# Kernel optimization log

Measured on AMD Instinct MI355X. Metric: run time of the kernel, lower is better.

The kernel has to match this reference:

```python
import jax, jax.numpy as jnp
import numpy as np

N_NODES = 50000
N_EDGES = 800000
F_IN = 256
HID = 64
HEADS = 4
NEG_SLOPE = 0.2


def setup_inputs() -> dict:
    key = jax.random.key(0)
    ks = jax.random.split(key, 12)
    x = jax.random.normal(ks[0], (N_NODES, F_IN), dtype=jnp.float32)
    src = jax.random.randint(ks[1], (N_EDGES,), 0, N_NODES)
    dst = jax.random.randint(ks[2], (N_EDGES,), 0, N_NODES)
    s0 = 1.0 / np.sqrt(F_IN)
    s1 = 1.0 / np.sqrt(HEADS * HID)
    W0 = jax.random.normal(ks[3], (F_IN, HEADS * HID), dtype=jnp.float32) * s0
    a_l0 = jax.random.normal(ks[4], (HEADS, HID), dtype=jnp.float32) * s1
    a_r0 = jax.random.normal(ks[5], (HEADS, HID), dtype=jnp.float32) * s1
    b0 = jnp.zeros((HEADS * HID,), dtype=jnp.float32)
    W1 = jax.random.normal(ks[6], (HEADS * HID, HEADS * HID), dtype=jnp.float32) * s1
    a_l1 = jax.random.normal(ks[7], (HEADS, HID), dtype=jnp.float32) * s1
    a_r1 = jax.random.normal(ks[8], (HEADS, HID), dtype=jnp.float32) * s1
    b1 = jnp.zeros((HEADS * HID,), dtype=jnp.float32)
    return {"x": x, "src": src, "dst": dst,
            "W0": W0, "a_l0": a_l0, "a_r0": a_r0, "b0": b0,
            "W1": W1, "a_l1": a_l1, "a_r1": a_r1, "b1": b1}


def _gat_layer(h, src, dst, W, a_l, a_r, b):
    # h: [N, F_in] -> feat: [N, H, D]
    feat = (h @ W).reshape(h.shape[0], HEADS, HID)
    el = jnp.sum(feat * a_l, axis=-1)  # [N, H]
    er = jnp.sum(feat * a_r, axis=-1)  # [N, H]
    e = jax.nn.leaky_relu(el[src] + er[dst], NEG_SLOPE)  # [E, H]
    # per-destination edge softmax (numerically stable)
    m = jax.ops.segment_max(e, dst, num_segments=N_NODES)  # [N, H]
    ex = jnp.exp(e - m[dst])
    s = jax.ops.segment_sum(ex, dst, num_segments=N_NODES)  # [N, H]
    alpha = ex / jnp.maximum(s[dst], 1e-9)  # [E, H]
    msg = feat[src] * alpha[:, :, None]  # [E, H, D]
    rst = jax.ops.segment_sum(msg, dst, num_segments=N_NODES)  # [N, H, D]
    rst = rst + b.reshape(1, HEADS, HID)
    return jax.nn.elu(rst)


def reference(x, src, dst, W0, a_l0, a_r0, b0, W1, a_l1, a_r1, b1):
    h = _gat_layer(x, src, dst, W0, a_l0, a_r0, b0)  # [N, H, D]
    h = h.reshape(N_NODES, HEADS * HID)              # flatten(1)
    h = _gat_layer(h, src, dst, W1, a_l1, a_r1, b1)  # [N, H, D]
    # list of per-head outputs h[:, i]
    return tuple(h[:, i] for i in range(HEADS))
```

## Files before the change

### kernel.cpp

```cpp
#include <hip/hip_runtime.h>
#include <math.h>

#define N_NODES 50000
#define N_EDGES 800000
#define HEADS 4
#define HID 64
#define FDIM 256
#define SCAN_CHUNK 1024
#define SCAN_NB ((N_NODES + SCAN_CHUNK - 1) / SCAN_CHUNK)

typedef __attribute__((ext_vector_type(8))) _Float16 half8;
typedef __attribute__((ext_vector_type(4))) _Float16 half4;
typedef __attribute__((ext_vector_type(4))) float f32x4;


__global__ __launch_bounds__(256) void scan_local(const int* __restrict__ counts,
                                                  int* __restrict__ offs,
                                                  int* __restrict__ bsum, int n) {
    __shared__ int part[256];
    const int b = blockIdx.x, t = threadIdx.x;
    const int base = b * SCAN_CHUNK + t * 4;
    int v[4];
#pragma unroll
    for (int j = 0; j < 4; j++) {
        int idx = base + j;
        v[j] = (idx < n) ? counts[idx] : 0;
    }
    int s0 = v[0], s1 = s0 + v[1], s2 = s1 + v[2], s3 = s2 + v[3];
    part[t] = s3;
    __syncthreads();
    for (int off = 1; off < 256; off <<= 1) {
        int x = (t >= off) ? part[t - off] : 0;
        __syncthreads();
        part[t] += x;
        __syncthreads();
    }
    int prefix = (t > 0) ? part[t - 1] : 0;
    int e[4] = {prefix, prefix + s0, prefix + s1, prefix + s2};
#pragma unroll
    for (int j = 0; j < 4; j++) {
        int idx = base + j;
        if (idx < n) offs[idx] = e[j];
    }
    if (t == 255) bsum[b] = part[255];
}

__global__ __launch_bounds__(64) void scan_bsum(int* __restrict__ bsum,
                                                int* __restrict__ offs, int nb, int n) {
    int lane = threadIdx.x;
    int own = (lane < nb) ? bsum[lane] : 0;
    int v = own;
    for (int off = 1; off < 64; off <<= 1) {
        int x = __shfl_up(v, off);
        if (lane >= off) v += x;
    }
    if (lane < nb) bsum[lane] = v - own;
    if (lane == nb - 1) offs[n] = v;
}

__global__ __launch_bounds__(256) void scan_add(int* __restrict__ offs,
                                                const int* __restrict__ bsum, int n) {
    const int b = blockIdx.x;
    const int p = bsum[b];
    const int base = b * SCAN_CHUNK + threadIdx.x * 4;
#pragma unroll
    for (int j = 0; j < 4; j++) {
        int idx = base + j;
        if (idx < n) offs[idx] += p;
    }
}

__global__ __launch_bounds__(256) void scatter_kernel(const int* __restrict__ src,
                                                      const int* __restrict__ dst,
                                                      const int* __restrict__ offs,
                                                      int* __restrict__ cursor,
                                                      int* __restrict__ csr_src, int E) {
    int i = blockIdx.x * blockDim.x + threadIdx.x;
    if (i < E) {
        int d = dst[i];
        int p = offs[d] + atomicAdd(&cursor[d], 1);
        csr_src[p] = src[i];
    }
}


__global__ __launch_bounds__(256) void wcast_kernel(const float* __restrict__ W0,
                                                    const float* __restrict__ W1,
                                                    _Float16* __restrict__ wt0,
                                                    _Float16* __restrict__ wt1) {
    const float* W = blockIdx.y ? W1 : W0;
    _Float16* wt = blockIdx.y ? wt1 : wt0;
    int n = blockIdx.x * 16 + (threadIdx.x >> 4);
    int k0 = (threadIdx.x & 15) * 16;
    for (int j = 0; j < 16; j++)
        wt[n * FDIM + k0 + j] = (_Float16)W[(k0 + j) * FDIM + n];
}

template <int A32, int DO_HIST>
__global__ __launch_bounds__(512) void mfma_gemm(const _Float16* __restrict__ A16,
                                                 const float* __restrict__ Af,
                                                 const _Float16* __restrict__ Bt,
                                                 const float* __restrict__ al,
                                                 const float* __restrict__ ar,
                                                 _Float16* __restrict__ feat16,
                                                 float* __restrict__ el,
                                                 float* __restrict__ er,
                                                 const int* __restrict__ dst,
                                                 int* __restrict__ counts) {
    __shared__ _Float16 ash[64 * 32];
    __shared__ _Float16 bsh[256 * 32];

    const int t = threadIdx.x;
    const int m0 = blockIdx.x * 64;
    const int wave = t >> 6, lane = t & 63;
    const int quad = lane >> 4, l16 = lane & 15;
    const int wr = (wave >> 2) * 32;
    const int wc = (wave & 3) * 64;

    if (DO_HIST) {
        for (int i = blockIdx.x * 512 + t; i < N_EDGES; i += gridDim.x * 512)
            atomicAdd(&counts[dst[i]], 1);
    }

    const f32x4 zero = {0.f, 0.f, 0.f, 0.f};
    f32x4 acc[2][4];
#pragma unroll
    for (int i = 0; i < 2; i++)
#pragma unroll
        for (int j = 0; j < 4; j++) acc[i][j] = zero;

    const int rslot = ((quad ^ (l16 & 3) ^ (l16 >> 2)) * 8);

    for (int kk = 0; kk < FDIM; kk += 32) {
        if (t < 256) {
            int row = t >> 2, slotL = t & 3;
            int ps = ((slotL ^ (row & 3) ^ ((row >> 2) & 3)) * 8);
            int gr = m0 + row; if (gr >= N_NODES) gr = N_NODES - 1;
            if (A32) {
                const float* p = &Af[(size_t)gr * FDIM + kk + slotL * 8];
                float4 f0 = *(const float4*)p;
                float4 f1 = *(const float4*)(p + 4);
                half8 hv = {(_Float16)f0.x, (_Float16)f0.y, (_Float16)f0.z, (_Float16)f0.w,
                            (_Float16)f1.x, (_Float16)f1.y, (_Float16)f1.z, (_Float16)f1.w};
                *(half8*)&ash[row * 32 + ps] = hv;
            } else {
                *(half8*)&ash[row * 32 + ps] =
                    *(const half8*)&A16[(size_t)gr * FDIM + kk + slotL * 8];
            }
        }
#pragma unroll
        for (int ii = 0; ii < 2; ii++) {
            int idx = t + ii * 512;
            int row = idx >> 2, slotL = idx & 3;
            int ps = ((slotL ^ (row & 3) ^ ((row >> 2) & 3)) * 8);
            *(half8*)&bsh[row * 32 + ps] =
                *(const half8*)&Bt[(size_t)row * FDIM + kk + slotL * 8];
        }
        __syncthreads();

        half8 af[2], bf[4];
#pragma unroll
        for (int i = 0; i < 2; i++)
            af[i] = *(half8*)&ash[(wr + i * 16 + l16) * 32 + rslot];
#pragma unroll
        for (int i = 0; i < 4; i++)
            bf[i] = *(half8*)&bsh[(wc + i * 16 + l16) * 32 + rslot];

#pragma unroll
        for (int mt = 0; mt < 2; mt++)
#pragma unroll
            for (int nt = 0; nt < 4; nt++)
                acc[mt][nt] = __builtin_amdgcn_mfma_f32_16x16x32_f16(bf[nt], af[mt], acc[mt][nt], 0, 0, 0);
        __syncthreads();
    }

    const int h = wc >> 6;
    float4 alv[4], arv[4];
#pragma unroll
    for (int nt = 0; nt < 4; nt++) {
        alv[nt] = *(const float4*)&al[wc + nt * 16 + quad * 4];
        arv[nt] = *(const float4*)&ar[wc + nt * 16 + quad * 4];
    }
#pragma unroll
    for (int mt = 0; mt < 2; mt++) {
        const int m = m0 + wr + mt * 16 + l16;
        const bool ok = (m < N_NODES);
        float pl = 0.f, pr = 0.f;
#pragma unroll
        for (int nt = 0; nt < 4; nt++) {
            f32x4 v = acc[mt][nt];
            if (ok) {
                half4 hv = {(_Float16)v[0], (_Float16)v[1], (_Float16)v[2], (_Float16)v[3]};
                *(half4*)&feat16[(size_t)m * FDIM + wc + nt * 16 + quad * 4] = hv;
            }
            pl += v[0] * alv[nt].x + v[1] * alv[nt].y + v[2] * alv[nt].z + v[3] * alv[nt].w;
            pr += v[0] * arv[nt].x + v[1] * arv[nt].y + v[2] * arv[nt].z + v[3] * arv[nt].w;
        }
        pl += __shfl_xor(pl, 16);
        pl += __shfl_xor(pl, 32);
        pr += __shfl_xor(pr, 16);
        pr += __shfl_xor(pr, 32);
        if (quad == 0 && ok) {
            el[m * 4 + h] = pl;
            er[m * 4 + h] = pr;
        }
    }
}

__global__ __launch_bounds__(256) void agg_fused(const _Float16* __restrict__ feat16,
                                                 const float* __restrict__ el,
                                                 const float* __restrict__ er,
                                                 const float* __restrict__ bias,
                                                 const int* __restrict__ offs,
                                                 const int* __restrict__ csr_src,
                                                 float* __restrict__ out,
                                                 _Float16* __restrict__ h1,
                                                 int mode) {
    const int wave = threadIdx.x >> 6;
    const int lane = threadIdx.x & 63;
    const int n = blockIdx.x * 4 + wave;
    const int head = lane >> 4;
    const int f = lane * 4;
    const int base16 = lane & 48;
    const int j16 = lane & 15;
    const int beg = offs[n];
    const int end = offs[n + 1];
    const float er_h = er[n * 4 + head];

    float4 acc = make_float4(0.f, 0.f, 0.f, 0.f);
    float ss = 0.f;

    for (int c = beg; c < end; c += 16) {
        int e = c + j16;
        int s_own = 0;
        float w_own = 0.f;
        if (e < end) {
            s_own = csr_src[e];
            float lg = el[s_own * 4 + head] + er_h;
            lg = (lg > 0.f) ? lg : 0.2f * lg;
            w_own = __expf(lg);
        }
        ss += w_own;

        int rem = end - c;
        if (rem > 16) rem = 16;

        int j = 0;
        for (; j + 3 < rem; j += 4) {
            int s0 = __shfl(s_own, base16 + j);
            int s1 = __shfl(s_own, base16 + j + 1);
            int s2 = __shfl(s_own, base16 + j + 2);
            int s3 = __shfl(s_own, base16 + j + 3);
            float w0 = __shfl(w_own, base16 + j);
            float w1 = __shfl(w_own, base16 + j + 1);
            float w2 = __shfl(w_own, base16 + j + 2);
            float w3 = __shfl(w_own, base16 + j + 3);
            half4 v0 = *(const half4*)&feat16[(size_t)s0 * FDIM + f];
            half4 v1 = *(const half4*)&feat16[(size_t)s1 * FDIM + f];
            half4 v2 = *(const half4*)&feat16[(size_t)s2 * FDIM + f];
            half4 v3 = *(const half4*)&feat16[(size_t)s3 * FDIM + f];
            acc.x += w0 * (float)v0[0] + w1 * (float)v1[0];
            acc.y += w0 * (float)v0[1] + w1 * (float)v1[1];
            acc.z += w0 * (float)v0[2] + w1 * (float)v1[2];
            acc.w += w0 * (float)v0[3] + w1 * (float)v1[3];
            acc.x += w2 * (float)v2[0] + w3 * (float)v3[0];
            acc.y += w2 * (float)v2[1] + w3 * (float)v3[1];
            acc.z += w2 * (float)v2[2] + w3 * (float)v3[2];
            acc.w += w2 * (float)v2[3] + w3 * (float)v3[3];
        }
        for (; j < rem; j++) {
            int s0 = __shfl(s_own, base16 + j);
            float w0 = __shfl(w_own, base16 + j);
            half4 v0 = *(const half4*)&feat16[(size_t)s0 * FDIM + f];
            acc.x += w0 * (float)v0[0];
            acc.y += w0 * (float)v0[1];
            acc.z += w0 * (float)v0[2];
            acc.w += w0 * (float)v0[3];
        }
    }

    ss += __shfl_xor(ss, 1, 16);
    ss += __shfl_xor(ss, 2, 16);
    ss += __shfl_xor(ss, 4, 16);
    ss += __shfl_xor(ss, 8, 16);

    float S = fmaxf(ss, 1e-9f);
    float inv = 1.f / S;
    float4 bv = *(const float4*)&bias[f];
    float r0 = acc.x * inv + bv.x;
    float r1 = acc.y * inv + bv.y;
    float r2 = acc.z * inv + bv.z;
    float r3 = acc.w * inv + bv.w;
    r0 = (r0 > 0.f) ? r0 : expm1f(r0);
    r1 = (r1 > 0.f) ? r1 : expm1f(r1);
    r2 = (r2 > 0.f) ? r2 : expm1f(r2);
    r3 = (r3 > 0.f) ? r3 : expm1f(r3);

    if (mode) {
        const int d = (lane & 15) * 4;
        float4 rv = make_float4(r0, r1, r2, r3);
        *(float4*)&out[(size_t)head * N_NODES * HID + (size_t)n * HID + d] = rv;
    } else {
        half4 hv = {(_Float16)r0, (_Float16)r1, (_Float16)r2, (_Float16)r3};
        *(half4*)&h1[(size_t)n * FDIM + f] = hv;
    }
}


extern "C" void kernel_launch(void* const* d_in, const int* in_sizes, int n_in,
                              void* d_out, int out_size, void* d_ws, size_t ws_size,
                              hipStream_t stream) {
    const float* x   = (const float*)d_in[0];
    const int*   src = (const int*)d_in[1];
    const int*   dst = (const int*)d_in[2];
    const float* W0  = (const float*)d_in[3];
    const float* al0 = (const float*)d_in[4];
    const float* ar0 = (const float*)d_in[5];
    const float* b0  = (const float*)d_in[6];
    const float* W1  = (const float*)d_in[7];
    const float* al1 = (const float*)d_in[8];
    const float* ar1 = (const float*)d_in[9];
    const float* b1  = (const float*)d_in[10];
    float* out = (float*)d_out;

    _Float16* h1 = (_Float16*)d_out;

    _Float16* feat16 = (_Float16*)d_ws;
    _Float16* wt0 = feat16 + (size_t)N_NODES * FDIM;
    _Float16* wt1 = wt0 + FDIM * FDIM;
    float* el    = (float*)(wt1 + FDIM * FDIM);
    float* er    = el + N_NODES * HEADS;
    int* counts  = (int*)(er + N_NODES * HEADS);
    int* cursor  = counts + N_NODES;
    int* offs    = cursor + N_NODES;
    int* bsum    = offs + 50016;
    int* csr_src = bsum + 64;

    const int ggrid = (N_NODES + 63) / 64;

    hipMemsetAsync(counts, 0, 2 * N_NODES * sizeof(int), stream);
    wcast_kernel<<<dim3(16, 2), 256, 0, stream>>>(W0, W1, wt0, wt1);

    mfma_gemm<1, 1><<<ggrid, 512, 0, stream>>>(nullptr, x, wt0, al0, ar0,
                                               feat16, el, er, dst, counts);

    scan_local<<<SCAN_NB, 256, 0, stream>>>(counts, offs, bsum, N_NODES);
    scan_bsum<<<1, 64, 0, stream>>>(bsum, offs, SCAN_NB, N_NODES);
    scan_add<<<SCAN_NB, 256, 0, stream>>>(offs, bsum, N_NODES);
    scatter_kernel<<<(N_EDGES + 255) / 256, 256, 0, stream>>>(src, dst, offs, cursor, csr_src, N_EDGES);

    agg_fused<<<N_NODES / 4, 256, 0, stream>>>(feat16, el, er, b0, offs, csr_src,
                                               out, h1, 0);

    mfma_gemm<0, 0><<<ggrid, 512, 0, stream>>>(h1, nullptr, wt1, al1, ar1,
                                               feat16, el, er, nullptr, nullptr);
    agg_fused<<<N_NODES / 4, 256, 0, stream>>>(feat16, el, er, b1, offs, csr_src,
                                               out, h1, 1);
}
```

Measured before the change: 367.4 us.

## Double-buffer GEMM LDS tiles with direct global-to-LDS async loads

The MFMA GEMM now keeps two LDS buffers for the A and B tiles and prefetches the next K-slice while the current one is being multiplied. B and fp16 A tiles are loaded with global_load_lds, which writes straight into LDS without passing through registers. The fp32 A path loads into registers early and converts after the MFMAs. The aim is to hide global-load latency and cut one barrier per iteration, at the cost of doubled LDS use, which may lower occupancy.

```diff
diff --git a/kernel.cpp b/kernel.cpp
--- a/kernel.cpp
+++ b/kernel.cpp
@@ -12,6 +12,11 @@
 typedef __attribute__((ext_vector_type(8))) _Float16 half8;
 typedef __attribute__((ext_vector_type(4))) _Float16 half4;
 typedef __attribute__((ext_vector_type(4))) float f32x4;
+
+__device__ __forceinline__ void gload_lds16(const void* g, void* l) {
+    __builtin_amdgcn_global_load_lds((const __attribute__((address_space(1))) void*)g,
+                                     (__attribute__((address_space(3))) void*)l, 16, 0, 0);
+}
 
 
 __global__ __launch_bounds__(256) void scan_local(const int* __restrict__ counts,
@@ -107,8 +112,8 @@
                                                  float* __restrict__ er,
                                                  const int* __restrict__ dst,
                                                  int* __restrict__ counts) {
-    __shared__ _Float16 ash[64 * 32];
-    __shared__ _Float16 bsh[256 * 32];
+    __shared__ _Float16 ash[2][64 * 32];
+    __shared__ _Float16 bsh[2][256 * 32];
 
     const int t = threadIdx.x;
     const int m0 = blockIdx.x * 64;
@@ -122,6 +127,12 @@
             atomicAdd(&counts[dst[i]], 1);
     }
 
+    const int arow = t >> 3, aq4 = t & 7;
+    const int agr = (m0 + arow < N_NODES) ? m0 + arow : N_NODES - 1;
+    const int aswz = (aq4 >> 1) ^ (arow & 3) ^ ((arow >> 2) & 3);
+    const int aoff = arow * 32 + aswz * 8 + (aq4 & 1) * 4;
+
+
     const f32x4 zero = {0.f, 0.f, 0.f, 0.f};
     f32x4 acc[2][4];
 #pragma unroll
@@ -129,49 +140,78 @@
 #pragma unroll
         for (int j = 0; j < 4; j++) acc[i][j] = zero;
 
-    const int rslot = ((quad ^ (l16 & 3) ^ (l16 >> 2)) * 8);
-
-    for (int kk = 0; kk < FDIM; kk += 32) {
-        if (t < 256) {
-            int row = t >> 2, slotL = t & 3;
-            int ps = ((slotL ^ (row & 3) ^ ((row >> 2) & 3)) * 8);
-            int gr = m0 + row; if (gr >= N_NODES) gr = N_NODES - 1;
+    const int rslot = (quad ^ (l16 & 3) ^ (l16 >> 2)) * 8;
+
+    float4 areg;
+
+    if (A32) {
+        const float* p = &Af[(size_t)agr * FDIM + aq4 * 4];
+        float4 f0 = *(const float4*)p;
+        half4 hv = {(_Float16)f0.x, (_Float16)f0.y, (_Float16)f0.z, (_Float16)f0.w};
+        *(half4*)&ash[0][aoff] = hv;
+    } else {
+        if (wave < 4) {
+            int u = wave * 64 + lane;
+            int row = u >> 2, sl = u & 3;
+            int ss = sl ^ (row & 3) ^ ((row >> 2) & 3);
+            int gr = (m0 + row < N_NODES) ? m0 + row : N_NODES - 1;
+            gload_lds16(&A16[(size_t)gr * FDIM + ss * 8], &ash[0][u * 8]);
+        }
+    }
+#pragma unroll
+    for (int ii = 0; ii < 2; ii++) {
+        int u = (wave * 2 + ii) * 64 + lane;
+        int row = u >> 2, sl = u & 3;
+        int ss = sl ^ (row & 3) ^ ((row >> 2) & 3);
+        gload_lds16(&Bt[(size_t)row * FDIM + ss * 8], &bsh[0][u * 8]);
+    }
+    __syncthreads();
+
+    for (int ks = 0; ks < 8; ks++) {
+        const int cur = ks & 1, nxt = cur ^ 1;
+        const int kk2 = (ks + 1) * 32;
+        const bool pf = (ks < 7);
+
+        if (pf) {
             if (A32) {
-                const float* p = &Af[(size_t)gr * FDIM + kk + slotL * 8];
-                float4 f0 = *(const float4*)p;
-                float4 f1 = *(const float4*)(p + 4);
-                half8 hv = {(_Float16)f0.x, (_Float16)f0.y, (_Float16)f0.z, (_Float16)f0.w,
-                            (_Float16)f1.x, (_Float16)f1.y, (_Float16)f1.z, (_Float16)f1.w};
-                *(half8*)&ash[row * 32 + ps] = hv;
+                areg = *(const float4*)&Af[(size_t)agr * FDIM + kk2 + aq4 * 4];
             } else {
-                *(half8*)&ash[row * 32 + ps] =
-                    *(const half8*)&A16[(size_t)gr * FDIM + kk + slotL * 8];
+                if (wave < 4) {
+                    int u = wave * 64 + lane;
+                    int row = u >> 2, sl = u & 3;
+                    int ss = sl ^ (row & 3) ^ ((row >> 2) & 3);
+                    int gr = (m0 + row < N_NODES) ? m0 + row : N_NODES - 1;
+                    gload_lds16(&A16[(size_t)gr * FDIM + kk2 + ss * 8], &ash[nxt][u * 8]);
+                }
             }
-        }
-#pragma unroll
-        for (int ii = 0; ii < 2; ii++) {
-            int idx = t + ii * 512;
-            int row = idx >> 2, slotL = idx & 3;
-            int ps = ((slotL ^ (row & 3) ^ ((row >> 2) & 3)) * 8);
-            *(half8*)&bsh[row * 32 + ps] =
-                *(const half8*)&Bt[(size_t)row * FDIM + kk + slotL * 8];
-        }
-        __syncthreads();
+#pragma unroll
+            for (int ii = 0; ii < 2; ii++) {
+                int u = (wave * 2 + ii) * 64 + lane;
+                int row = u >> 2, sl = u & 3;
+                int ss = sl ^ (row & 3) ^ ((row >> 2) & 3);
+                gload_lds16(&Bt[(size_t)row * FDIM + kk2 + ss * 8], &bsh[nxt][u * 8]);
+            }
+        }
 
         half8 af[2], bf[4];
 #pragma unroll
         for (int i = 0; i < 2; i++)
-            af[i] = *(half8*)&ash[(wr + i * 16 + l16) * 32 + rslot];
+            af[i] = *(half8*)&ash[cur][(wr + i * 16 + l16) * 32 + rslot];
 #pragma unroll
         for (int i = 0; i < 4; i++)
-            bf[i] = *(half8*)&bsh[(wc + i * 16 + l16) * 32 + rslot];
+            bf[i] = *(half8*)&bsh[cur][(wc + i * 16 + l16) * 32 + rslot];
 
 #pragma unroll
         for (int mt = 0; mt < 2; mt++)
 #pragma unroll
             for (int nt = 0; nt < 4; nt++)
                 acc[mt][nt] = __builtin_amdgcn_mfma_f32_16x16x32_f16(bf[nt], af[mt], acc[mt][nt], 0, 0, 0);
-        __syncthreads();
+
+        if (A32 && pf) {
+            half4 hv = {(_Float16)areg.x, (_Float16)areg.y, (_Float16)areg.z, (_Float16)areg.w};
+            *(half4*)&ash[nxt][aoff] = hv;
+        }
+        if (pf) __syncthreads();
     }
 
     const int h = wc >> 6;
```

New measurement: 366.8 us. No clear change (-0.2%).
